# Kernel optimization log

Hardware: AMD Instinct MI355X
Metric: run time of the kernel (lower is better)

Reference implementation:

```python
import jax, jax.numpy as jnp
import numpy as np

B = 2048; E = 6; H = 4; D = 128; DH = D // H
LTXT = 24; CS = 20; JD = 7; SD = 16; LD = 32; K = 2
NLB = 4; NLD = 3; VOCAB = 512; DFF = 4 * D


def _ln(x, s, b, eps=1e-5):
    m = x.mean(-1, keepdims=True)
    v = ((x - m) ** 2).mean(-1, keepdims=True)
    return (x - m) * jax.lax.rsqrt(v + eps) * s + b


def _mha(xq, xkv, Wqkv, bqkv, Wo, bo, key_pad=None):
    # torch nn.MultiheadAttention, batch_first, eval (no dropout)
    Wq, Wk, Wv = jnp.split(Wqkv, 3, axis=-1)
    bq, bk, bv = jnp.split(bqkv, 3)
    Bc, Lq, _ = xq.shape
    Lk = xkv.shape[1]
    q = (xq @ Wq + bq).reshape(Bc, Lq, H, DH)
    k = (xkv @ Wk + bk).reshape(Bc, Lk, H, DH)
    v = (xkv @ Wv + bv).reshape(Bc, Lk, H, DH)
    s = jnp.einsum('bqhd,bkhd->bhqk', q, k) * (1.0 / DH ** 0.5)
    if key_pad is not None:
        s = jnp.where(key_pad[:, None, None, :], -1e9, s)
    a = jax.nn.softmax(s, axis=-1)
    o = jnp.einsum('bhqk,bkhd->bqhd', a, v).reshape(Bc, Lq, D)
    return o @ Wo + bo


def _sinusoidal_pe(L, d):
    pos = jnp.arange(L, dtype=jnp.float32)[:, None]
    div = jnp.exp(jnp.arange(0, d, 2, dtype=jnp.float32) * (-np.log(10000.0) / d))
    pe = jnp.zeros((L, d), jnp.float32)
    pe = pe.at[:, 0::2].set(jnp.sin(pos * div))
    return pe.at[:, 1::2].set(jnp.cos(pos * div))


def _forward(ids, state, tok_emb, pos_emb, bert_Wqkv, bert_bqkv, bert_Wo, bert_bo, bert_W1, bert_b1, bert_W2, bert_b2, bert_ln_s, bert_ln_b, bert_lnf_s, bert_lnf_b, se_W1, se_b1, se_W2, se_b2, se_ln_s, se_ln_b, r_W1, r_b1, r_W2, r_b2, r_ln_s, r_ln_b, gate_W, gate_b, exp_sp_W, exp_sp_b, exp_zp_W, exp_zp_b, exp_attn_Wqkv, exp_attn_bqkv, exp_attn_Wo, exp_attn_bo, exp_ln_s, exp_ln_b, exp_ff_W1, exp_ff_b1, exp_ff_W2, exp_ff_b2, exp_head_W, exp_head_b):
    Bc = ids.shape[0]
    gelu = lambda t: jax.nn.gelu(t, approximate=False)
    # ---- MiniBERT (post-LN encoder) ----
    pad = ids == 0  # PAD token
    x = tok_emb[ids] + pos_emb[None]  # [B,24,128]
    for l in range(NLB):
        a = _mha(x, x, bert_Wqkv[l], bert_bqkv[l], bert_Wo[l], bert_bo[l], pad)
        x = _ln(x + a, bert_ln_s[l, 0], bert_ln_b[l, 0])
        h = gelu(x @ bert_W1[l] + bert_b1[l]) @ bert_W2[l] + bert_b2[l]
        x = _ln(x + h, bert_ln_s[l, 1], bert_ln_b[l, 1])
    intent = _ln(x, bert_lnf_s, bert_lnf_b)[:, 0]  # CLS embedding [B,128]
    # ---- StateEncoder (MLP + LN) ----
    semb = _ln(gelu(state @ se_W1 + se_b1) @ se_W2 + se_b2, se_ln_s, se_ln_b)
    # ---- FusionRouter: top-k gating ----
    fused = _ln(gelu(jnp.concatenate([intent, semb], -1) @ r_W1 + r_b1) @ r_W2 + r_b2, r_ln_s, r_ln_b)
    logits = fused @ gate_W + gate_b  # [B,6]
    all_probs = jax.nn.softmax(logits, axis=-1)
    tv, ti = jax.lax.top_k(logits, K)
    weights = jax.nn.softmax(tv, axis=-1)  # [B,2]
    # ---- ACTExperts, inference path (z = 0) ----
    qpe = _sinusoidal_pe(CS, D)
    z = jnp.zeros((Bc, LD), state.dtype)

    def one_expert(sp_W, sp_b, zp_W, zp_b, aW, ab, oW, ob, lns, lnb, fW1, fb1, fW2, fb2, hW, hb):
        mem = jnp.stack([state @ sp_W + sp_b, z @ zp_W + zp_b], axis=1)  # [B,2,128]
        xq = jnp.broadcast_to(qpe[None], (Bc, CS, D))
        for l in range(NLD):  # norm_first decoder layers, relu FFN
            xn = _ln(xq, lns[l, 0], lnb[l, 0])
            xq = xq + _mha(xn, xn, aW[l, 0], ab[l, 0], oW[l, 0], ob[l, 0])
            xn = _ln(xq, lns[l, 1], lnb[l, 1])
            xq = xq + _mha(xn, mem, aW[l, 1], ab[l, 1], oW[l, 1], ob[l, 1])
            xn = _ln(xq, lns[l, 2], lnb[l, 2])
            xq = xq + jax.nn.relu(xn @ fW1[l] + fb1[l]) @ fW2[l] + fb2[l]
        return xq @ hW + hb  # [B,20,7]

    outs = jax.vmap(one_expert)(exp_sp_W, exp_sp_b, exp_zp_W, exp_zp_b, exp_attn_Wqkv, exp_attn_bqkv, exp_attn_Wo, exp_attn_bo, exp_ln_s, exp_ln_b, exp_ff_W1, exp_ff_b1, exp_ff_W2, exp_ff_b2, exp_head_W, exp_head_b)  # [E,B,20,7]
    # scatter top-k weights to a dense [B,E] gate and combine expert outputs
    w_full = jnp.zeros((Bc, E), logits.dtype).at[jnp.arange(Bc)[:, None], ti].add(weights)
    return jnp.einsum('be,ebtj->btj', w_full, outs)


def setup_inputs() -> dict:
    key = jax.random.key(0)
    it = iter(jax.random.split(key, 64))
    w = lambda *shape: jax.random.normal(next(it), shape, jnp.float32) * 0.05
    inp = {}
    inp['ids'] = jax.random.randint(next(it), (B, LTXT), 0, VOCAB, dtype=jnp.int32)
    inp['state'] = jax.random.normal(next(it), (B, SD), jnp.float32)
    inp['tok_emb'] = w(VOCAB, D).at[0].set(0.0)  # padding_idx=0
    inp['pos_emb'] = w(LTXT, D)
    inp['bert_Wqkv'] = w(NLB, D, 3 * D); inp['bert_bqkv'] = jnp.zeros((NLB, 3 * D))
    inp['bert_Wo'] = w(NLB, D, D); inp['bert_bo'] = jnp.zeros((NLB, D))
    inp['bert_W1'] = w(NLB, D, DFF); inp['bert_b1'] = jnp.zeros((NLB, DFF))
    inp['bert_W2'] = w(NLB, DFF, D); inp['bert_b2'] = jnp.zeros((NLB, D))
    inp['bert_ln_s'] = jnp.ones((NLB, 2, D)); inp['bert_ln_b'] = jnp.zeros((NLB, 2, D))
    inp['bert_lnf_s'] = jnp.ones((D,)); inp['bert_lnf_b'] = jnp.zeros((D,))
    inp['se_W1'] = w(SD, D); inp['se_b1'] = jnp.zeros((D,))
    inp['se_W2'] = w(D, D); inp['se_b2'] = jnp.zeros((D,))
    inp['se_ln_s'] = jnp.ones((D,)); inp['se_ln_b'] = jnp.zeros((D,))
    inp['r_W1'] = w(2 * D, D); inp['r_b1'] = jnp.zeros((D,))
    inp['r_W2'] = w(D, D); inp['r_b2'] = jnp.zeros((D,))
    inp['r_ln_s'] = jnp.ones((D,)); inp['r_ln_b'] = jnp.zeros((D,))
    inp['gate_W'] = w(D, E) * 10.0  # non-degenerate routing (source inits zeros)
    inp['gate_b'] = jnp.zeros((E,))
    inp['exp_sp_W'] = w(E, SD, D); inp['exp_sp_b'] = jnp.zeros((E, D))
    inp['exp_zp_W'] = w(E, LD, D); inp['exp_zp_b'] = jnp.zeros((E, D))
    inp['exp_attn_Wqkv'] = w(E, NLD, 2, D, 3 * D); inp['exp_attn_bqkv'] = jnp.zeros((E, NLD, 2, 3 * D))
    inp['exp_attn_Wo'] = w(E, NLD, 2, D, D); inp['exp_attn_bo'] = jnp.zeros((E, NLD, 2, D))
    inp['exp_ln_s'] = jnp.ones((E, NLD, 3, D)); inp['exp_ln_b'] = jnp.zeros((E, NLD, 3, D))
    inp['exp_ff_W1'] = w(E, NLD, D, DFF); inp['exp_ff_b1'] = jnp.zeros((E, NLD, DFF))
    inp['exp_ff_W2'] = w(E, NLD, DFF, D); inp['exp_ff_b2'] = jnp.zeros((E, NLD, D))
    inp['exp_head_W'] = w(E, D, JD); inp['exp_head_b'] = jnp.zeros((E, JD))
    return inp


def reference(ids, state, tok_emb, pos_emb, bert_Wqkv, bert_bqkv, bert_Wo, bert_bo, bert_W1, bert_b1, bert_W2, bert_b2, bert_ln_s, bert_ln_b, bert_lnf_s, bert_lnf_b, se_W1, se_b1, se_W2, se_b2, se_ln_s, se_ln_b, r_W1, r_b1, r_W2, r_b2, r_ln_s, r_ln_b, gate_W, gate_b, exp_sp_W, exp_sp_b, exp_zp_W, exp_zp_b, exp_attn_Wqkv, exp_attn_bqkv, exp_attn_Wo, exp_attn_bo, exp_ln_s, exp_ln_b, exp_ff_W1, exp_ff_b1, exp_ff_W2, exp_ff_b2, exp_head_W, exp_head_b):
    return _forward(ids, state, tok_emb, pos_emb, bert_Wqkv, bert_bqkv, bert_Wo, bert_bo, bert_W1, bert_b1, bert_W2, bert_b2, bert_ln_s, bert_ln_b, bert_lnf_s, bert_lnf_b, se_W1, se_b1, se_W2, se_b2, se_ln_s, se_ln_b, r_W1, r_b1, r_W2, r_b2, r_ln_s, r_ln_b, gate_W, gate_b, exp_sp_W, exp_sp_b, exp_zp_W, exp_zp_b, exp_attn_Wqkv, exp_attn_bqkv, exp_attn_Wo, exp_attn_bo, exp_ln_s, exp_ln_b, exp_ff_W1, exp_ff_b1, exp_ff_W2, exp_ff_b2, exp_head_W, exp_head_b)
```

## Files before the change

kernel.cpp:

```cpp
#include <hip/hip_runtime.h>
#include <math.h>

#define DEVI __device__ __forceinline__

namespace {

constexpr int Bn   = 2048;
constexpr int En   = 6;
constexpr int Hn   = 4;
constexpr int Dn   = 128;
constexpr int DHn  = 32;
constexpr int LTn  = 24;
constexpr int CSn  = 20;
constexpr int JDn  = 7;
constexpr int SDn  = 16;
constexpr int NLBn = 4;
constexpr int NLDn = 3;
constexpr int DFFn = 512;
constexpr float INV_SQRT_DH = 0.17677669529663687f;

constexpr int PAIRS  = 4096;
constexpr int MPMAX  = PAIRS * 20 + En * 128;
constexpr int NBGMAX = PAIRS * 20 / 128 + En;
constexpr int GEXP_OFF = 64;
// ... 253 lines not shown
    for (int q = 0; q < 4; ++q) {
      s1[q] = v[0][q] + v[1][q];
      s2[q] = v[0][q] * v[0][q] + v[1][q] * v[1][q];
    }
#pragma unroll
    for (int o = 1; o < 16; o <<= 1)
#pragma unroll
      for (int q = 0; q < 4; ++q) { s1[q] += __shfl_xor(s1[q], o); s2[q] += __shfl_xor(s2[q], o); }
    if (r0 == 0)
#pragma unroll
      for (int q = 0; q < 4; ++q) { red[g * 4 + q][wv][0] = s1[q]; red[g * 4 + q][wv][1] = s2[q]; }
    __syncthreads();
#pragma unroll
    for (int q = 0; q < 4; ++q) {
      const int r = g * 4 + q;
      const float t1 = red[r][0][0] + red[r][1][0] + red[r][2][0] + red[r][3][0];
      const float t2 = red[r][0][1] + red[r][1][1] + red[r][2][1] + red[r][3][1];
      const float m  = t1 * (1.f / 128.f);
      const float rs = rsqrtf(t2 * (1.f / 128.f) - m * m + 1e-5f);
      const int row = mtg * 16 + r;
#pragma unroll
      for (int i = 0; i < 2; ++i) {
        const int col = (wv * 2 + i) * 16 + r0;
        const float o = (v[i][q] - m) * rs * gs[col] + gb[col];
        X[(size_t)row * 128 + col] = o;
        short hh, ll; split2(o, hh, ll);
        const size_t pk = apos(row, col, 4);
        OAh[pk] = hh; OAl[pk] = ll;
      }
    }
    __syncthreads();
  }
}

__global__ __launch_bounds__(256) void bw1_kernel(
    const short* __restrict__ Ah, const short* __restrict__ Al,
    const short* __restrict__ Bp, const float* __restrict__ bias,
    short* __restrict__ Hh, short* __restrict__ Hl)
{
  const int mt0 = (int)blockIdx.x * 4;
  const int nc  = (int)blockIdx.y;
  const int lane = (int)threadIdx.x & 63, wv = (int)threadIdx.x >> 6;
  const int r0 = lane & 15, g = lane >> 4;
  short8 bh[2][4], bl[2][4];
#pragma unroll
  for (int i = 0; i < 2; ++i)
#pragma unroll
    for (int kt = 0; kt < 4; ++kt) {
      const short* tb = Bp + (((size_t)(nc * 8 + wv * 2 + i) * 4 + kt) << 10);
      bh[i][kt] = *reinterpret_cast<const short8*>(tb + lane * 8);
      bl[i][kt] = *reinterpret_cast<const short8*>(tb + 512 + lane * 8);
    }
#pragma unroll 2
  for (int mt = 0; mt < 4; ++mt) {
    const int mtg = mt0 + mt;
    short8 ah[4], al[4];
#pragma unroll
    for (int kt = 0; kt < 4; ++kt) {
      ah[kt] = *reinterpret_cast<const short8*>(Ah + (((size_t)mtg * 4 + kt) * 64 + lane) * 8);
      al[kt] = *reinterpret_cast<const short8*>(Al + (((size_t)mtg * 4 + kt) * 64 + lane) * 8);
    }
#pragma unroll
    for (int i = 0; i < 2; ++i) {
      f32x4v c = {0.f, 0.f, 0.f, 0.f};
#pragma unroll
      for (int kt = 0; kt < 4; ++kt) {
        c = __builtin_amdgcn_mfma_f32_16x16x32_bf16(ah[kt], bh[i][kt], c, 0, 0, 0);
        c = __builtin_amdgcn_mfma_f32_16x16x32_bf16(al[kt], bh[i][kt], c, 0, 0, 0);
        c = __builtin_amdgcn_mfma_f32_16x16x32_bf16(ah[kt], bl[i][kt], c, 0, 0, 0);
      }
      const int col = nc * 128 + (wv * 2 + i) * 16 + r0;
      const float bb = bias[col];
#pragma unroll
      for (int q = 0; q < 4; ++q) {
        const int row = mtg * 16 + g * 4 + q;
        short hh, ll; split2(geluf(c[q] + bb), hh, ll);
        const size_t pk = apos(row, col, 16);
        Hh[pk] = hh; Hl[pk] = ll;
      }
    }
  }
}

__global__ __launch_bounds__(512) void bw2a_kernel(
    const short* __restrict__ Hh, const short* __restrict__ Hl,
    const short* __restrict__ Bp, const float* __restrict__ bias,
    float* __restrict__ X)
{
  const int mt0 = (int)blockIdx.x * 4;
  const int lane = (int)threadIdx.x & 63, wv = (int)threadIdx.x >> 6;
  const int r0 = lane & 15, g = lane >> 4;
  short8 bh[8], bl[8];
#pragma unroll
  for (int kk = 0; kk < 8; ++kk) {
    const short* tb = Bp + (((size_t)wv * 16 + kk) << 10);
    bh[kk] = *reinterpret_cast<const short8*>(tb + lane * 8);
    bl[kk] = *reinterpret_cast<const short8*>(tb + 512 + lane * 8);
  }
#pragma unroll 2
  for (int mt = 0; mt < 4; ++mt) {
    const int mtg = mt0 + mt;
    f32x4v c = {0.f, 0.f, 0.f, 0.f};
#pragma unroll
    for (int kk = 0; kk < 8; ++kk) {
      const short8 ah = *reinterpret_cast<const short8*>(Hh + (((size_t)mtg * 16 + kk) * 64 + lane) * 8);
      const short8 al = *reinterpret_cast<const short8*>(Hl + (((size_t)mtg * 16 + kk) * 64 + lane) * 8);
      c = __builtin_amdgcn_mfma_f32_16x16x32_bf16(ah, bh[kk], c, 0, 0, 0);
      c = __builtin_amdgcn_mfma_f32_16x16x32_bf16(al, bh[kk], c, 0, 0, 0);
      c = __builtin_amdgcn_mfma_f32_16x16x32_bf16(ah, bl[kk], c, 0, 0, 0);
    }
    const int col = wv * 16 + r0;
    const float bb = bias[col];
#pragma unroll
    for (int q = 0; q < 4; ++q)
      X[(size_t)(mtg * 16 + g * 4 + q) * 128 + col] += c[q] + bb;
  }
}

__global__ __launch_bounds__(512) void bw2b_kernel(
    const short* __restrict__ Hh, const short* __restrict__ Hl,
    const short* __restrict__ Bp, const float* __restrict__ gs,
    const float* __restrict__ gb, float* __restrict__ X,
    short* __restrict__ OAh, short* __restrict__ OAl)
{
  __shared__ float red[16][8][2];
  const int mt0 = (int)blockIdx.x * 4;
  const int lane = (int)threadIdx.x & 63, wv = (int)threadIdx.x >> 6;
  const int r0 = lane & 15, g = lane >> 4;
  short8 bh[8], bl[8];
#pragma unroll
  for (int kk = 0; kk < 8; ++kk) {
    const short* tb = Bp + (((size_t)wv * 16 + 8 + kk) << 10);
    bh[kk] = *reinterpret_cast<const short8*>(tb + lane * 8);
    bl[kk] = *reinterpret_cast<const short8*>(tb + 512 + lane * 8);
  }
  for (int mt = 0; mt < 4; ++mt) {
    const int mtg = mt0 + mt;
    f32x4v c = {0.f, 0.f, 0.f, 0.f};
#pragma unroll
    for (int kk = 0; kk < 8; ++kk) {
      const short8 ah = *reinterpret_cast<const short8*>(Hh + (((size_t)mtg * 16 + 8 + kk) * 64 + lane) * 8);
      const short8 al = *reinterpret_cast<const short8*>(Hl + (((size_t)mtg * 16 + 8 + kk) * 64 + lane) * 8);
      c = __builtin_amdgcn_mfma_f32_16x16x32_bf16(ah, bh[kk], c, 0, 0, 0);
      c = __builtin_amdgcn_mfma_f32_16x16x32_bf16(al, bh[kk], c, 0, 0, 0);
      c = __builtin_amdgcn_mfma_f32_16x16x32_bf16(ah, bl[kk], c, 0, 0, 0);
    }
    const int col = wv * 16 + r0;
    float v[4], s1[4], s2[4];
#pragma unroll
    for (int q = 0; q < 4; ++q) {
      const int row = mtg * 16 + g * 4 + q;
      v[q] = c[q] + X[(size_t)row * 128 + col];
      s1[q] = v[q]; s2[q] = v[q] * v[q];
    }
#pragma unroll
    for (int o = 1; o < 16; o <<= 1)
#pragma unroll
      for (int q = 0; q < 4; ++q) { s1[q] += __shfl_xor(s1[q], o); s2[q] += __shfl_xor(s2[q], o); }
    if (r0 == 0)
#pragma unroll
      for (int q = 0; q < 4; ++q) { red[g * 4 + q][wv][0] = s1[q]; red[g * 4 + q][wv][1] = s2[q]; }
    __syncthreads();
#pragma unroll
    for (int q = 0; q < 4; ++q) {
      const int r = g * 4 + q;
      float t1 = 0.f, t2 = 0.f;
#pragma unroll
      for (int w = 0; w < 8; ++w) { t1 += red[r][w][0]; t2 += red[r][w][1]; }
      const float m  = t1 * (1.f / 128.f);
      const float rs = rsqrtf(t2 * (1.f / 128.f) - m * m + 1e-5f);
      const int row = mtg * 16 + r;
      const float o = (v[q] - m) * rs * gs[col] + gb[col];
      X[(size_t)row * 128 + col] = o;
      short hh, ll; split2(o, hh, ll);
      const size_t pk = apos(row, col, 4);
      OAh[pk] = hh; OAl[pk] = ll;
    }
    __syncthreads();
  }
}

__global__ __launch_bounds__(256) void bintent_kernel(
    const float* __restrict__ X, const float* __restrict__ lnf_s,
    const float* __restrict__ lnf_b, float* __restrict__ intent)
{
  const int w = (int)threadIdx.x >> 6, lane = (int)threadIdx.x & 63;
  const int b = (int)blockIdx.x * 4 + w;
  const float* xr = X + (size_t)b * LTn * 128;
  const float a0 = xr[lane], a1 = xr[lane + 64];
  float s1 = a0 + a1, s2 = a0 * a0 + a1 * a1;
#pragma unroll
  for (int o = 32; o > 0; o >>= 1) { s1 += __shfl_xor(s1, o); s2 += __shfl_xor(s2, o); }
  const float m  = s1 * (1.f / 128.f);
  const float rs = rsqrtf(s2 * (1.f / 128.f) - m * m + 1e-5f);
  intent[b * 128 + lane]      = (a0 - m) * rs * lnf_s[lane]      + lnf_b[lane];
  intent[b * 128 + lane + 64] = (a1 - m) * rs * lnf_s[lane + 64] + lnf_b[lane + 64];
}

struct RouterP {
  const float* state; const float* intent;
  const float* se_W1; const float* se_b1; const float* se_W2; const float* se_b2;
  const float* se_ln_s; const float* se_ln_b;
  const float* r_W1; const float* r_b1; const float* r_W2; const float* r_b2;
  const float* r_ln_s; const float* r_ln_b;
  const float* gate_W; const float* gate_b;
  int* ridx; float* rwgt;
};

DEVI void ln128(float* x, const float* gs, const float* gb, float* red)
{
  const int c = (int)threadIdx.x;
  const float a = x[c];
  float s1 = a, s2 = a * a;
#pragma unroll
  for (int o = 32; o > 0; o >>= 1) { s1 += __shfl_xor(s1, o); s2 += __shfl_xor(s2, o); }
  const int wid = c >> 6;
  if ((c & 63) == 0) { red[wid * 2] = s1; red[wid * 2 + 1] = s2; }
  __syncthreads();
  s1 = red[0] + red[2]; s2 = red[1] + red[3];
  const float m  = s1 * (1.f / 128.f);
  const float rs = rsqrtf(s2 * (1.f / 128.f) - m * m + 1e-5f);
  __syncthreads();
  x[c] = (a - m) * rs * gs[c] + gb[c];
}

DEVI float dot128i(const float* __restrict__ h, const float* __restrict__ W,
                   const int c, const int wstr)
{
  float a0 = 0.f, a1 = 0.f, a2 = 0.f, a3 = 0.f;
#pragma unroll 8
  for (int k = 0; k < 128; k += 4) {
    a0 = fmaf(h[k + 0], W[(k + 0) * wstr + c], a0);
    a1 = fmaf(h[k + 1], W[(k + 1) * wstr + c], a1);
    a2 = fmaf(h[k + 2], W[(k + 2) * wstr + c], a2);
    a3 = fmaf(h[k + 3], W[(k + 3) * wstr + c], a3);
// ... 151 lines not shown
__global__ __launch_bounds__(256) void compose_kernel(
    const float* __restrict__ sp_W, const float* __restrict__ sp_b,
    const float* __restrict__ zp_b, const float* __restrict__ aW,
    const float* __restrict__ ab,
    float* __restrict__ C, float* __restrict__ k0c, float* __restrict__ k1c)
{
  const int li = (int)blockIdx.x;
  const int ex = li / NLDn;
  const int c2 = (int)threadIdx.x;
  const float* W   = aW + (size_t)(li * 2 + 1) * Dn * 384 + Dn;
  const float* bb  = ab + (size_t)(li * 2 + 1) * 384 + Dn;
  const float* spw = sp_W + ex * SDn * Dn;
  const float* spb = sp_b + ex * Dn;
  const float* zpb = zp_b + ex * Dn;
  float acc[SDn];
#pragma unroll
  for (int k = 0; k < SDn; ++k) acc[k] = 0.f;
  float a0 = 0.f, a1 = 0.f;
  for (int d = 0; d < Dn; ++d) {
    const float w = W[(size_t)d * 384 + c2];
#pragma unroll
    for (int k = 0; k < SDn; ++k) acc[k] = fmaf(spw[k * Dn + d], w, acc[k]);
    a0 = fmaf(spb[d], w, a0);
    a1 = fmaf(zpb[d], w, a1);
  }
#pragma unroll
  for (int k = 0; k < SDn; ++k) C[((size_t)li * SDn + k) * 256 + c2] = acc[k];
  k0c[li * 256 + c2] = bb[c2] + a0;
  k1c[li * 256 + c2] = bb[c2] + a1;
}

template<int NTW, int EPI, bool HASB>
__global__ __launch_bounds__(256) void gemm_k128(
    const short* __restrict__ A, const short* __restrict__ Bb, const int strideB,
    const float* __restrict__ biasb, const int strideBias, const int ntOff,
    short* __restrict__ OutBf, const int obstr, short* __restrict__ OutP,
    const float* __restrict__ lnsA, const float* __restrict__ lnbA, const int subOff,
    float* __restrict__ X, const int* __restrict__ sch)
{
  __shared__ float red[16][4][2];
  const int k = (int)blockIdx.x;
  if (k >= sch[0]) return;
  const int ex  = sch[GEXP_OFF + k];
  const int mt0 = sch[GMT_OFF + k];
  const short* Bp = Bb + (size_t)ex * strideB;
  const float* bias = biasb + (size_t)ex * strideBias;
  const float* gs = (EPI == 4) ? lnsA + ex * (NLDn * 3 * 128) + subOff : nullptr;
  const float* gb = (EPI == 4) ? lnbA + ex * (NLDn * 3 * 128) + subOff : nullptr;
  const int lane = (int)threadIdx.x & 63, wv = (int)threadIdx.x >> 6;
  const int r0 = lane & 15, g = lane >> 4;
  short8 bf[NTW][4];
#pragma unroll
  for (int i = 0; i < NTW; ++i)
#pragma unroll
    for (int kt = 0; kt < 4; ++kt)
      bf[i][kt] = *reinterpret_cast<const short8*>(
          Bp + (((size_t)(ntOff + wv * NTW + i) * 4 + kt) * 64 + lane) * 8);
  for (int mt = 0; mt < 8; ++mt) {
    short8 a[4];
#pragma unroll
    for (int kt = 0; kt < 4; ++kt)
      a[kt] = *reinterpret_cast<const short8*>(
          A + (((size_t)(mt0 + mt) * 4 + kt) * 64 + lane) * 8);
    float v[NTW][4];
#pragma unroll
    for (int i = 0; i < NTW; ++i) {
      f32x4v c = {0.f, 0.f, 0.f, 0.f};
#pragma unroll
      for (int kt = 0; kt < 4; ++kt)
        c = __builtin_amdgcn_mfma_f32_16x16x32_bf16(a[kt], bf[i][kt], c, 0, 0, 0);
      const int colL = (wv * NTW + i) * 16 + r0;
      const float bb = HASB ? bias[colL] : 0.f;
      const int rowB = (mt0 + mt) * 16 + g * 4;
#pragma unroll
      for (int q = 0; q < 4; ++q) {
        const int row = rowB + q;
        const float val = c[q] + bb;
        if (EPI == 0) {
          OutBf[(size_t)row * obstr + colL] = f2bf(val);
        } else if (EPI == 3) {
          const float rv = fmaxf(val, 0.f);
          const int j = colL >> 3, kt2 = j >> 2, g2 = j & 3;
          const int lp = g2 * 16 + (row & 15);
          OutP[(((size_t)(row >> 4) * 8 + kt2) * 64 + lp) * 8 + (colL & 7)] = f2bf(rv);
        } else {
          v[i][q] = val + X[(size_t)row * 128 + colL];
        }
      }
    }
    if (EPI == 4) {
      static_assert(EPI != 4 || NTW == 2, "fused LN requires NTW==2");
      float s1[4], s2[4];
#pragma unroll
      for (int q = 0; q < 4; ++q) {
        s1[q] = v[0][q] + v[1][q];
        s2[q] = v[0][q] * v[0][q] + v[1][q] * v[1][q];
      }
#pragma unroll
      for (int o = 1; o < 16; o <<= 1)
#pragma unroll
        for (int q = 0; q < 4; ++q) { s1[q] += __shfl_xor(s1[q], o); s2[q] += __shfl_xor(s2[q], o); }
      if (r0 == 0)
#pragma unroll
        for (int q = 0; q < 4; ++q) { red[g * 4 + q][wv][0] = s1[q]; red[g * 4 + q][wv][1] = s2[q]; }
      __syncthreads();
#pragma unroll
      for (int q = 0; q < 4; ++q) {
        const int r = g * 4 + q;
        const float t1 = red[r][0][0] + red[r][1][0] + red[r][2][0] + red[r][3][0];
        const float t2 = red[r][0][1] + red[r][1][1] + red[r][2][1] + red[r][3][1];
        const float m  = t1 * (1.f / 128.f);
        const float rs = rsqrtf(t2 * (1.f / 128.f) - m * m + 1e-5f);
        const int row = (mt0 + mt) * 16 + r;
#pragma unroll
        for (int i = 0; i < 2; ++i) {
          const int col = (wv * 2 + i) * 16 + r0;
          const float o = (v[i][q] - m) * rs * gs[col] + gb[col];
          X[(size_t)row * 128 + col] = v[i][q];
          OutP[apos(row, col, 4)] = f2bf(o);
        }
      }
      __syncthreads();
    }
  }
}

template<bool HASB, bool DOLN>
__global__ __launch_bounds__(256) void gemm_k256(
    const short* __restrict__ A, const short* __restrict__ Bb, const int strideB,
    const float* __restrict__ biasb, const int strideBias, const int ktOff,
    float* __restrict__ X, short* __restrict__ OutP,
    const float* __restrict__ lnsA, const float* __restrict__ lnbA, const int subOff,
    const int* __restrict__ sch)
{
  __shared__ float red[16][4][2];
  const int k = (int)blockIdx.x;
  if (k >= sch[0]) return;
  const int ex  = sch[GEXP_OFF + k];
  const int mt0 = sch[GMT_OFF + k];
  const short* Bp = Bb + (size_t)ex * strideB;
  const float* bias = biasb + (size_t)ex * strideBias;
  const float* gs = DOLN ? lnsA + ex * (NLDn * 3 * 128) + subOff : nullptr;
  const float* gb = DOLN ? lnbA + ex * (NLDn * 3 * 128) + subOff : nullptr;
  const int lane = (int)threadIdx.x & 63, wv = (int)threadIdx.x >> 6;
  const int r0 = lane & 15, g = lane >> 4;
  short8 bf[2][8];
#pragma unroll
  for (int i = 0; i < 2; ++i)
#pragma unroll
    for (int kk = 0; kk < 8; ++kk)
      bf[i][kk] = *reinterpret_cast<const short8*>(
          Bp + (((size_t)(wv * 2 + i) * 16 + ktOff + kk) * 64 + lane) * 8);
  for (int mt = 0; mt < 8; ++mt) {
    short8 a[8];
#pragma unroll
    for (int kk = 0; kk < 8; ++kk)
      a[kk] = *reinterpret_cast<const short8*>(
          A + (((size_t)(mt0 + mt) * 8 + kk) * 64 + lane) * 8);
    float v[2][4];
#pragma unroll
    for (int i = 0; i < 2; ++i) {
      f32x4v c = {0.f, 0.f, 0.f, 0.f};
#pragma unroll
      for (int kk = 0; kk < 8; ++kk)
        c = __builtin_amdgcn_mfma_f32_16x16x32_bf16(a[kk], bf[i][kk], c, 0, 0, 0);
      const int colL = (wv * 2 + i) * 16 + r0;
      const float bb = HASB ? bias[colL] : 0.f;
      const int rowB = (mt0 + mt) * 16 + g * 4;
#pragma unroll
      for (int q = 0; q < 4; ++q) {
        const int row = rowB + q;
        if (DOLN) v[i][q] = c[q] + bb + X[(size_t)row * 128 + colL];
        else      X[(size_t)row * 128 + colL] += c[q] + bb;
      }
    }
    if (DOLN) {
      float s1[4], s2[4];
#pragma unroll
      for (int q = 0; q < 4; ++q) {
        s1[q] = v[0][q] + v[1][q];
        s2[q] = v[0][q] * v[0][q] + v[1][q] * v[1][q];
      }
#pragma unroll
      for (int o = 1; o < 16; o <<= 1)
#pragma unroll
        for (int q = 0; q < 4; ++q) { s1[q] += __shfl_xor(s1[q], o); s2[q] += __shfl_xor(s2[q], o); }
      if (r0 == 0)
#pragma unroll
        for (int q = 0; q < 4; ++q) { red[g * 4 + q][wv][0] = s1[q]; red[g * 4 + q][wv][1] = s2[q]; }
      __syncthreads();
#pragma unroll
      for (int q = 0; q < 4; ++q) {
        const int r = g * 4 + q;
        const float t1 = red[r][0][0] + red[r][1][0] + red[r][2][0] + red[r][3][0];
        const float t2 = red[r][0][1] + red[r][1][1] + red[r][2][1] + red[r][3][1];
        const float m  = t1 * (1.f / 128.f);
        const float rs = rsqrtf(t2 * (1.f / 128.f) - m * m + 1e-5f);
        const int row = (mt0 + mt) * 16 + r;
#pragma unroll
        for (int i = 0; i < 2; ++i) {
          const int col = (wv * 2 + i) * 16 + r0;
          const float o = (v[i][q] - m) * rs * gs[col] + gb[col];
          X[(size_t)row * 128 + col] = v[i][q];
          OutP[apos(row, col, 4)] = f2bf(o);
        }
      }
      __syncthreads();
    }
  }
}

__global__ __launch_bounds__(64) void sattn_kernel(
    const short* __restrict__ QKVb, const int* __restrict__ prow,
    short* __restrict__ ANP)
{
  __shared__ float qs[CSn * HSTR], ks[CSn * HSTR], vs[CSn * HSTR];
  __shared__ float att[CSn * CSn];
  const int i = (int)blockIdx.x, h = (int)blockIdx.y;
  const int tid = (int)threadIdx.x;
  const int row0 = prow[i];
  for (int u = tid; u < CSn * 12; u += 64) {
    const int il = u / 12, r = u % 12, which = r >> 2, d8 = r & 3;
    const short8 s = *reinterpret_cast<const short8*>(
        QKVb + (size_t)(row0 + il) * 384 + which * 128 + h * 32 + d8 * 8);
    float* dst = (which == 0 ? qs : which == 1 ? ks : vs) + il * HSTR + d8 * 8;
#pragma unroll
    for (int u8 = 0; u8 < 8; ++u8) dst[u8] = bf2f(s[u8]);
  }
  __syncthreads();
  for (int e = tid; e < CSn * CSn; e += 64) {
    const int ii = e / CSn, j = e % CSn;
    const float* qp = qs + ii * HSTR;
    const float* kp = ks + j * HSTR;
    float acc = 0.f;
#pragma unroll
    for (int d = 0; d < DHn; d += 4) {
      const float4 qa = *reinterpret_cast<const float4*>(qp + d);
      const float4 kb = *reinterpret_cast<const float4*>(kp + d);
      acc += qa.x * kb.x + qa.y * kb.y + qa.z * kb.z + qa.w * kb.w;
    }
    att[e] = acc * INV_SQRT_DH;
  }
  __syncthreads();
  if (tid < CSn) {
    float* row = att + tid * CSn;
    float m = row[0];
#pragma unroll 4
    for (int j = 1; j < CSn; ++j) m = fmaxf(m, row[j]);
    float s = 0.f;
#pragma unroll 4
    for (int j = 0; j < CSn; ++j) { const float ex = expf(row[j] - m); row[j] = ex; s += ex; }
    const float inv = 1.f / s;
#pragma unroll 4
    for (int j = 0; j < CSn; ++j) row[j] *= inv;
  }
  __syncthreads();
  for (int e = tid; e < CSn * 32; e += 64) {
    const int ii = e >> 5, c = e & 31;
    const float* arow = att + ii * CSn;
    float acc = 0.f;
#pragma unroll 4
    for (int j = 0; j < CSn; ++j) acc = fmaf(arow[j], vs[j * HSTR + c], acc);
    ANP[apos(row0 + ii, h * 32 + c, 4)] = f2bf(acc);
  }
}

__global__ __launch_bounds__(256) void cattn_kernel(
    const short* __restrict__ Qb, const float* __restrict__ state,
    const float* __restrict__ C, const float* __restrict__ k0c,
    const float* __restrict__ k1c, const int layer,
    const int* __restrict__ plist, const int* __restrict__ prow,
    const int* __restrict__ pexp, short* __restrict__ ANP)
{
  __shared__ float q[CSn * Dn];
  __shared__ float memkv[2 * 256];
  __shared__ float catt[2 * Hn * CSn];
  __shared__ float st[SDn];
  const int i = (int)blockIdx.x;
  const int ex = pexp[i];
  const int b = plist[i] >> 1;
  const int li = ex * NLDn + layer;
  const int row0 = prow[i];
  const int tid = (int)threadIdx.x;

  if (tid < SDn) st[tid] = state[b * SDn + tid];
  for (int e8 = tid; e8 < CSn * 16; e8 += 256) {
    const int il = e8 >> 4, c8 = e8 & 15;
    const short8 s = *reinterpret_cast<const short8*>(
        Qb + (size_t)(row0 + il) * 128 + c8 * 8);
    float* dst = q + il * Dn + c8 * 8;
// ... 112 lines not shown
  float* rwgt   = (float*)alloc(PAIRS * 4);
  short* pQ     = (short*)alloc((size_t)36 * 49152 * 2);
  short* pO     = (short*)alloc((size_t)36 * 16384 * 2);
  short* pF1    = (short*)alloc((size_t)18 * 65536 * 2);
  short* pF2    = (short*)alloc((size_t)18 * 65536 * 2);
  short* pbQ    = (short*)alloc((size_t)4 * 98304 * 2);
  short* pbO    = (short*)alloc((size_t)4 * 32768 * 2);
  short* pbW1   = (short*)alloc((size_t)4 * 131072 * 2);
  short* pbW2   = (short*)alloc((size_t)4 * 131072 * 2);
  int*   sch    = (int*)  alloc(2048 * 4);
  int*   plist  = (int*)  alloc(PAIRS * 4);
  int*   prow   = (int*)  alloc(PAIRS * 4);
  int*   pexp   = (int*)  alloc(PAIRS * 4);
  int*   ppos   = (int*)  alloc(PAIRS * 4);
  float* Cmat   = (float*)alloc((size_t)18 * SDn * 256 * 4);
  float* k0c    = (float*)alloc((size_t)18 * 256 * 4);
  float* k1c    = (float*)alloc((size_t)18 * 256 * 4);
  constexpr size_t ARENA_BYTES = 192806912;
  char* arena = alloc(ARENA_BYTES);
  if ((size_t)(cur - (char*)d_ws) > ws_size) return;

  float* Xb  = (float*)(arena);
  short* Ah  = (short*)(arena + 25165824);
  short* Al  = (short*)(arena + 37748736);
  float* SBb = (float*)(arena + 50331648);
  short* Hh  = (short*)(arena + 50331648);
  short* Hl  = (short*)(arena + 100663296);
  float* X2   = (float*)(arena);
  short* ANP  = (short*)(arena + 42336256);
  short* SBh  = (short*)(arena + 63504384);
  float* Rbuf = (float*)(arena + 190513152);

  qpe_kernel<<<dim3(10), dim3(256), 0, stream>>>(qpe);

  {
    const int tq = 36 * 6144;
    pack_kernel<<<dim3((tq + 255) / 256), dim3(256), 0, stream>>>(
        (const float*)d_in[34], pQ, 128, 384, tq);
    const int to = 36 * 2048;
    pack_kernel<<<dim3((to + 255) / 256), dim3(256), 0, stream>>>(
        (const float*)d_in[36], pO, 128, 128, to);
    const int t1c = 18 * 8192;
    pack_kernel<<<dim3((t1c + 255) / 256), dim3(256), 0, stream>>>(
        (const float*)d_in[40], pF1, 128, 512, t1c);
    const int t2c = 18 * 8192;
    pack_kernel<<<dim3((t2c + 255) / 256), dim3(256), 0, stream>>>(
        (const float*)d_in[42], pF2, 512, 128, t2c);
    const int bq = 4 * 6144;
    pack2_kernel<<<dim3((bq + 255) / 256), dim3(256), 0, stream>>>(
        (const float*)d_in[4], pbQ, 128, 384, bq);
    const int bo = 4 * 2048;
    pack2_kernel<<<dim3((bo + 255) / 256), dim3(256), 0, stream>>>(
        (const float*)d_in[6], pbO, 128, 128, bo);
    const int bw1 = 4 * 8192;
    pack2_kernel<<<dim3((bw1 + 255) / 256), dim3(256), 0, stream>>>(
        (const float*)d_in[8], pbW1, 128, 512, bw1);
    const int bw2 = 4 * 8192;
    pack2_kernel<<<dim3((bw2 + 255) / 256), dim3(256), 0, stream>>>(
        (const float*)d_in[10], pbW2, 512, 128, bw2);
    compose_kernel<<<dim3(En * NLDn), dim3(256), 0, stream>>>(
        (const float*)d_in[30], (const float*)d_in[31], (const float*)d_in[33],
        (const float*)d_in[34], (const float*)d_in[35], Cmat, k0c, k1c);
  }

  {
    const float* bq  = (const float*)d_in[5];
    const float* bo  = (const float*)d_in[7];
    const float* b1  = (const float*)d_in[9];
    const float* b2  = (const float*)d_in[11];
    const float* lns = (const float*)d_in[12];
    const float* lnb = (const float*)d_in[13];

    bembed_kernel<<<dim3(ROWSB / 16), dim3(256), 0, stream>>>(
        ids, tok_emb, pos_emb, Xb, Ah, Al);
    for (int l = 0; l < NLBn; ++l) {
      bqkv_kernel<<<dim3(ROWSB / 64, 3), dim3(256), 0, stream>>>(
          Ah, Al, pbQ + (size_t)l * 98304, bq + l * 384, SBb);
      battn_kernel<<<dim3(Bn, Hn), dim3(64), 0, stream>>>(SBb, ids, Ah, Al);
      bo_ln_kernel<<<dim3(ROWSB / 64), dim3(256), 0, stream>>>(
          Ah, Al, pbO + (size_t)l * 32768, bo + l * 128,
          lns + l * 256, lnb + l * 256, Xb, Ah, Al);
      bw1_kernel<<<dim3(ROWSB / 64, 4), dim3(256), 0, stream>>>(
          Ah, Al, pbW1 + (size_t)l * 131072, b1 + l * 512, Hh, Hl);
      bw2a_kernel<<<dim3(ROWSB / 64), dim3(512), 0, stream>>>(
          Hh, Hl, pbW2 + (size_t)l * 131072, b2 + l * 128, Xb);
      bw2b_kernel<<<dim3(ROWSB / 64), dim3(512), 0, stream>>>(
          Hh, Hl, pbW2 + (size_t)l * 131072,
          lns + l * 256 + 128, lnb + l * 256 + 128, Xb, Ah, Al);
    }
    bintent_kernel<<<dim3(Bn / 4), dim3(256), 0, stream>>>(
        Xb, (const float*)d_in[14], (const float*)d_in[15], intent);
  }

  {
    RouterP rp;
    rp.state = state; rp.intent = intent;
    rp.se_W1 = (const float*)d_in[16]; rp.se_b1 = (const float*)d_in[17];
    rp.se_W2 = (const float*)d_in[18]; rp.se_b2 = (const float*)d_in[19];
    rp.se_ln_s = (const float*)d_in[20]; rp.se_ln_b = (const float*)d_in[21];
    rp.r_W1 = (const float*)d_in[22]; rp.r_b1 = (const float*)d_in[23];
    rp.r_W2 = (const float*)d_in[24]; rp.r_b2 = (const float*)d_in[25];
    rp.r_ln_s = (const float*)d_in[26]; rp.r_ln_b = (const float*)d_in[27];
    rp.gate_W = (const float*)d_in[28]; rp.gate_b = (const float*)d_in[29];
    rp.ridx = ridx; rp.rwgt = rwgt;
    router_kernel<<<dim3(Bn), dim3(128), 0, stream>>>(rp);
  }

  const float* ab   = (const float*)d_in[35];
  const float* abo  = (const float*)d_in[37];
  const float* lnsA = (const float*)d_in[38];
  const float* lnbA = (const float*)d_in[39];
  const float* fb1A = (const float*)d_in[41];
  const float* fb2A = (const float*)d_in[43];
  const float* hW   = (const float*)d_in[44];
  const float* hB   = (const float*)d_in[45];

  {
    sched_kernel<<<dim3(1), dim3(256), 0, stream>>>(ridx, sch, plist, prow, pexp, ppos);
    xinit_kernel<<<dim3(MPMAX * 32 / 256), dim3(256), 0, stream>>>(qpe, sch, X2);
    ln_pack_kernel<<<dim3(MPMAX / 16), dim3(256), 0, stream>>>(
        X2, ANP, lnsA, lnbA, 0, sch);
    short* HP = SBh;
    for (int l = 0; l < NLDn; ++l) {
      gemm_k128<6, 0, true><<<dim3(NBGMAX), dim3(256), 0, stream>>>(
          ANP, pQ + (l * 2 + 0) * 49152, 294912,
          ab + (l * 2 + 0) * 384, 2304, 0,
          SBh, 384, nullptr, nullptr, nullptr, 0, nullptr, sch);
      sattn_kernel<<<dim3(PAIRS, Hn), dim3(64), 0, stream>>>(SBh, prow, ANP);
      gemm_k128<2, 4, true><<<dim3(NBGMAX), dim3(256), 0, stream>>>(
          ANP, pO + (l * 2 + 0) * 16384, 98304,
          abo + (l * 2 + 0) * 128, 768, 0,
          nullptr, 0, ANP, lnsA, lnbA, (l * 3 + 1) * 128, X2, sch);
      gemm_k128<2, 0, true><<<dim3(NBGMAX), dim3(256), 0, stream>>>(
          ANP, pQ + (l * 2 + 1) * 49152, 294912,
          ab + (l * 2 + 1) * 384, 2304, 0,
          SBh, 128, nullptr, nullptr, nullptr, 0, nullptr, sch);
      cattn_kernel<<<dim3(PAIRS), dim3(256), 0, stream>>>(
          SBh, state, Cmat, k0c, k1c, l, plist, prow, pexp, ANP);
      gemm_k128<2, 4, true><<<dim3(NBGMAX), dim3(256), 0, stream>>>(
          ANP, pO + (l * 2 + 1) * 16384, 98304,
          abo + (l * 2 + 1) * 128, 768, 0,
          nullptr, 0, ANP, lnsA, lnbA, (l * 3 + 2) * 128, X2, sch);
      gemm_k128<4, 3, true><<<dim3(NBGMAX), dim3(256), 0, stream>>>(
          ANP, pF1 + l * 65536, 196608,
          fb1A + l * 512 + 0 * 256, 1536, 0,
          nullptr, 0, HP, nullptr, nullptr, 0, nullptr, sch);
      gemm_k256<true, false><<<dim3(NBGMAX), dim3(256), 0, stream>>>(
          HP, pF2 + l * 65536, 196608, fb2A + l * 128, 384, 0,
          X2, nullptr, nullptr, nullptr, 0, sch);
      gemm_k128<4, 3, true><<<dim3(NBGMAX), dim3(256), 0, stream>>>(
          ANP, pF1 + l * 65536, 196608,
          fb1A + l * 512 + 1 * 256, 1536, 16,
          nullptr, 0, HP, nullptr, nullptr, 0, nullptr, sch);
      if (l < NLDn - 1) {
        gemm_k256<false, true><<<dim3(NBGMAX), dim3(256), 0, stream>>>(
            HP, pF2 + l * 65536, 196608, fb2A + l * 128, 384, 8,
            X2, ANP, lnsA, lnbA, ((l + 1) * 3 + 0) * 128, sch);
      } else {
        gemm_k256<false, false><<<dim3(NBGMAX), dim3(256), 0, stream>>>(
            HP, pF2 + l * 65536, 196608, fb2A + l * 128, 384, 8,
            X2, nullptr, nullptr, nullptr, 0, sch);
      }
    }
    head_kernel<<<dim3(PAIRS), dim3(256), 0, stream>>>(
        X2, plist, prow, pexp, rwgt, hW, hB, Rbuf);
    combine_kernel<<<dim3((Bn * 140 + 255) / 256), dim3(256), 0, stream>>>(
        Rbuf, ppos, (float*)d_out);
  }
}
```

Baseline: 1.714 ms.

## Fuse split-K FFN second GEMM halves into single kernels for BERT and experts

The BERT FFN down-projection was split into two kernels over K halves (one accumulating into X, one adding and applying LayerNorm); they are merged into one kernel that loops over both K halves while holding accumulators for four M tiles in registers. The expert FFN path gets the same treatment: the two K=256 GEMM launches become one K=512 kernel, and the first up-projection GEMM now writes into a wider 16-tile H buffer via an ntOff offset. This removes a launch and a full read-modify-write of X per layer, at the cost of more live accumulator registers and a reordered launch sequence.

Measured after the change: 1.688 ms. No clear change (-1.5%).

```diff
diff --git a/kernel.cpp b/kernel.cpp
--- a/kernel.cpp
+++ b/kernel.cpp
@@ -359,75 +359,52 @@
   }
 }
 
-__global__ __launch_bounds__(512) void bw2a_kernel(
+__global__ __launch_bounds__(512) void bw2_kernel(
     const short* __restrict__ Hh, const short* __restrict__ Hl,
     const short* __restrict__ Bp, const float* __restrict__ bias,
-    float* __restrict__ X)
-{
-  const int mt0 = (int)blockIdx.x * 4;
-  const int lane = (int)threadIdx.x & 63, wv = (int)threadIdx.x >> 6;
-  const int r0 = lane & 15, g = lane >> 4;
-  short8 bh[8], bl[8];
-#pragma unroll
-  for (int kk = 0; kk < 8; ++kk) {
-    const short* tb = Bp + (((size_t)wv * 16 + kk) << 10);
-    bh[kk] = *reinterpret_cast<const short8*>(tb + lane * 8);
-    bl[kk] = *reinterpret_cast<const short8*>(tb + 512 + lane * 8);
-  }
-#pragma unroll 2
-  for (int mt = 0; mt < 4; ++mt) {
-    const int mtg = mt0 + mt;
-    f32x4v c = {0.f, 0.f, 0.f, 0.f};
-#pragma unroll
-    for (int kk = 0; kk < 8; ++kk) {
-      const short8 ah = *reinterpret_cast<const short8*>(Hh + (((size_t)mtg * 16 + kk) * 64 + lane) * 8);
-      const short8 al = *reinterpret_cast<const short8*>(Hl + (((size_t)mtg * 16 + kk) * 64 + lane) * 8);
-      c = __builtin_amdgcn_mfma_f32_16x16x32_bf16(ah, bh[kk], c, 0, 0, 0);
-      c = __builtin_amdgcn_mfma_f32_16x16x32_bf16(al, bh[kk], c, 0, 0, 0);
-      c = __builtin_amdgcn_mfma_f32_16x16x32_bf16(ah, bl[kk], c, 0, 0, 0);
-    }
-    const int col = wv * 16 + r0;
-    const float bb = bias[col];
-#pragma unroll
-    for (int q = 0; q < 4; ++q)
-      X[(size_t)(mtg * 16 + g * 4 + q) * 128 + col] += c[q] + bb;
-  }
-}
-
-__global__ __launch_bounds__(512) void bw2b_kernel(
-    const short* __restrict__ Hh, const short* __restrict__ Hl,
-    const short* __restrict__ Bp, const float* __restrict__ gs,
-    const float* __restrict__ gb, float* __restrict__ X,
-    short* __restrict__ OAh, short* __restrict__ OAl)
+    const float* __restrict__ gs, const float* __restrict__ gb,
+    float* __restrict__ X, short* __restrict__ OAh, short* __restrict__ OAl)
 {
   __shared__ float red[16][8][2];
   const int mt0 = (int)blockIdx.x * 4;
   const int lane = (int)threadIdx.x & 63, wv = (int)threadIdx.x >> 6;
   const int r0 = lane & 15, g = lane >> 4;
-  short8 bh[8], bl[8];
-#pragma unroll
-  for (int kk = 0; kk < 8; ++kk) {
-    const short* tb = Bp + (((size_t)wv * 16 + 8 + kk) << 10);
-    bh[kk] = *reinterpret_cast<const short8*>(tb + lane * 8);
-    bl[kk] = *reinterpret_cast<const short8*>(tb + 512 + lane * 8);
-  }
+  f32x4v c[4];
+#pragma unroll
+  for (int mt = 0; mt < 4; ++mt) c[mt] = (f32x4v){0.f, 0.f, 0.f, 0.f};
+#pragma unroll
+  for (int half = 0; half < 2; ++half) {
+    short8 bh[8], bl[8];
+#pragma unroll
+    for (int kk = 0; kk < 8; ++kk) {
+      const short* tb = Bp + (((size_t)(wv * 16 + half * 8 + kk)) << 10);
+      bh[kk] = *reinterpret_cast<const short8*>(tb + lane * 8);
+      bl[kk] = *reinterpret_cast<const short8*>(tb + 512 + lane * 8);
+    }
+#pragma unroll
+    for (int mt = 0; mt < 4; ++mt) {
+      const int mtg = mt0 + mt;
+#pragma unroll
+      for (int kk = 0; kk < 8; ++kk) {
+        const short8 ah = *reinterpret_cast<const short8*>(
+            Hh + (((size_t)mtg * 16 + half * 8 + kk) * 64 + lane) * 8);
+        const short8 al = *reinterpret_cast<const short8*>(
+            Hl + (((size_t)mtg * 16 + half * 8 + kk) * 64 + lane) * 8);
+        c[mt] = __builtin_amdgcn_mfma_f32_16x16x32_bf16(ah, bh[kk], c[mt], 0, 0, 0);
+        c[mt] = __builtin_amdgcn_mfma_f32_16x16x32_bf16(al, bh[kk], c[mt], 0, 0, 0);
+        c[mt] = __builtin_amdgcn_mfma_f32_16x16x32_bf16(ah, bl[kk], c[mt], 0, 0, 0);
+      }
+    }
+  }
+  const int col = wv * 16 + r0;
+  const float bb = bias[col];
   for (int mt = 0; mt < 4; ++mt) {
     const int mtg = mt0 + mt;
-    f32x4v c = {0.f, 0.f, 0.f, 0.f};
-#pragma unroll
-    for (int kk = 0; kk < 8; ++kk) {
-      const short8 ah = *reinterpret_cast<const short8*>(Hh + (((size_t)mtg * 16 + 8 + kk) * 64 + lane) * 8);
-      const short8 al = *reinterpret_cast<const short8*>(Hl + (((size_t)mtg * 16 + 8 + kk) * 64 + lane) * 8);
-      c = __builtin_amdgcn_mfma_f32_16x16x32_bf16(ah, bh[kk], c, 0, 0, 0);
-      c = __builtin_amdgcn_mfma_f32_16x16x32_bf16(al, bh[kk], c, 0, 0, 0);
-      c = __builtin_amdgcn_mfma_f32_16x16x32_bf16(ah, bl[kk], c, 0, 0, 0);
-    }
-    const int col = wv * 16 + r0;
     float v[4], s1[4], s2[4];
 #pragma unroll
     for (int q = 0; q < 4; ++q) {
       const int row = mtg * 16 + g * 4 + q;
-      v[q] = c[q] + X[(size_t)row * 128 + col];
+      v[q] = c[mt][q] + bb + X[(size_t)row * 128 + col];
       s1[q] = v[q]; s2[q] = v[q] * v[q];
     }
 #pragma unroll
@@ -745,14 +722,14 @@
           const float rv = fmaxf(val, 0.f);
           const int j = colL >> 3, kt2 = j >> 2, g2 = j & 3;
           const int lp = g2 * 16 + (row & 15);
-          OutP[(((size_t)(row >> 4) * 8 + kt2) * 64 + lp) * 8 + (colL & 7)] = f2bf(rv);
+          OutP[(((size_t)(row >> 4) * 16 + (ntOff >> 1) + kt2) * 64 + lp) * 8 + (colL & 7)]
+              = f2bf(rv);
         } else {
           v[i][q] = val + X[(size_t)row * 128 + colL];
         }
       }
     }
     if (EPI == 4) {
-      static_assert(EPI != 4 || NTW == 2, "fused LN requires NTW==2");
       float s1[4], s2[4];
 #pragma unroll
       for (int q = 0; q < 4; ++q) {
@@ -788,10 +765,10 @@
   }
 }
 
-template<bool HASB, bool DOLN>
-__global__ __launch_bounds__(256) void gemm_k256(
+template<bool DOLN>
+__global__ __launch_bounds__(256) void gemm_k256f(
     const short* __restrict__ A, const short* __restrict__ Bb, const int strideB,
-    const float* __restrict__ biasb, const int strideBias, const int ktOff,
+    const float* __restrict__ biasb, const int strideBias,
     float* __restrict__ X, short* __restrict__ OutP,
     const float* __restrict__ lnsA, const float* __restrict__ lnbA, const int subOff,
     const int* __restrict__ sch)
@@ -807,68 +784,94 @@
   const float* gb = DOLN ? lnbA + ex * (NLDn * 3 * 128) + subOff : nullptr;
   const int lane = (int)threadIdx.x & 63, wv = (int)threadIdx.x >> 6;
   const int r0 = lane & 15, g = lane >> 4;
-  short8 bf[2][8];
-#pragma unroll
-  for (int i = 0; i < 2; ++i)
-#pragma unroll
-    for (int kk = 0; kk < 8; ++kk)
-      bf[i][kk] = *reinterpret_cast<const short8*>(
-          Bp + (((size_t)(wv * 2 + i) * 16 + ktOff + kk) * 64 + lane) * 8);
-  for (int mt = 0; mt < 8; ++mt) {
-    short8 a[8];
-#pragma unroll
-    for (int kk = 0; kk < 8; ++kk)
-      a[kk] = *reinterpret_cast<const short8*>(
-          A + (((size_t)(mt0 + mt) * 8 + kk) * 64 + lane) * 8);
-    float v[2][4];
-#pragma unroll
-    for (int i = 0; i < 2; ++i) {
-      f32x4v c = {0.f, 0.f, 0.f, 0.f};
-#pragma unroll
-      for (int kk = 0; kk < 8; ++kk)
-        c = __builtin_amdgcn_mfma_f32_16x16x32_bf16(a[kk], bf[i][kk], c, 0, 0, 0);
-      const int colL = (wv * 2 + i) * 16 + r0;
-      const float bb = HASB ? bias[colL] : 0.f;
-      const int rowB = (mt0 + mt) * 16 + g * 4;
-#pragma unroll
-      for (int q = 0; q < 4; ++q) {
-        const int row = rowB + q;
-        if (DOLN) v[i][q] = c[q] + bb + X[(size_t)row * 128 + colL];
-        else      X[(size_t)row * 128 + colL] += c[q] + bb;
-      }
-    }
-    if (DOLN) {
-      float s1[4], s2[4];
-#pragma unroll
-      for (int q = 0; q < 4; ++q) {
-        s1[q] = v[0][q] + v[1][q];
-        s2[q] = v[0][q] * v[0][q] + v[1][q] * v[1][q];
-      }
-#pragma unroll
-      for (int o = 1; o < 16; o <<= 1)
-#pragma unroll
-        for (int q = 0; q < 4; ++q) { s1[q] += __shfl_xor(s1[q], o); s2[q] += __shfl_xor(s2[q], o); }
-      if (r0 == 0)
-#pragma unroll
-        for (int q = 0; q < 4; ++q) { red[g * 4 + q][wv][0] = s1[q]; red[g * 4 + q][wv][1] = s2[q]; }
-      __syncthreads();
-#pragma unroll
-      for (int q = 0; q < 4; ++q) {
-        const int r = g * 4 + q;
-        const float t1 = red[r][0][0] + red[r][1][0] + red[r][2][0] + red[r][3][0];
-        const float t2 = red[r][0][1] + red[r][1][1] + red[r][2][1] + red[r][3][1];
-        const float m  = t1 * (1.f / 128.f);
-        const float rs = rsqrtf(t2 * (1.f / 128.f) - m * m + 1e-5f);
-        const int row = (mt0 + mt) * 16 + r;
+#pragma unroll
+  for (int mc = 0; mc < 2; ++mc) {
+    f32x4v c[4][2];
+#pragma unroll
+    for (int mtl = 0; mtl < 4; ++mtl)
+#pragma unroll
+      for (int i = 0; i < 2; ++i) c[mtl][i] = (f32x4v){0.f, 0.f, 0.f, 0.f};
+#pragma unroll
+    for (int half = 0; half < 2; ++half) {
+      short8 bf[2][8];
+#pragma unroll
+      for (int i = 0; i < 2; ++i)
+#pragma unroll
+        for (int kk = 0; kk < 8; ++kk)
+          bf[i][kk] = *reinterpret_cast<const short8*>(
+              Bp + (((size_t)(wv * 2 + i) * 16 + half * 8 + kk) * 64 + lane) * 8);
+#pragma unroll
+      for (int mtl = 0; mtl < 4; ++mtl) {
+        const int mtg = mt0 + mc * 4 + mtl;
+        short8 a[8];
+#pragma unroll
+        for (int kk = 0; kk < 8; ++kk)
+          a[kk] = *reinterpret_cast<const short8*>(
+              A + (((size_t)mtg * 16 + half * 8 + kk) * 64 + lane) * 8);
+#pragma unroll
+        for (int i = 0; i < 2; ++i)
+#pragma unroll
+          for (int kk = 0; kk < 8; ++kk)
+            c[mtl][i] = __builtin_amdgcn_mfma_f32_16x16x32_bf16(a[kk], bf[i][kk], c[mtl][i], 0, 0, 0);
+      }
+    }
+#pragma unroll
+    for (int mtl = 0; mtl < 4; ++mtl) {
+      const int mtg = mt0 + mc * 4 + mtl;
+      float v[2][4];
+#pragma unroll
+      for (int i = 0; i < 2; ++i) {
+        const int colL = (wv * 2 + i) * 16 + r0;
+        const float bb = bias[colL];
+#pragma unroll
+        for (int q = 0; q < 4; ++q) {
+          const int row = mtg * 16 + g * 4 + q;
+          v[i][q] = c[mtl][i][q] + bb + X[(size_t)row * 128 + colL];
+        }
+      }
+      if (DOLN) {
+        float s1[4], s2[4];
+#pragma unroll
+        for (int q = 0; q < 4; ++q) {
+          s1[q] = v[0][q] + v[1][q];
+          s2[q] = v[0][q] * v[0][q] + v[1][q] * v[1][q];
+        }
+#pragma unroll
+        for (int o = 1; o < 16; o <<= 1)
+#pragma unroll
+          for (int q = 0; q < 4; ++q) { s1[q] += __shfl_xor(s1[q], o); s2[q] += __shfl_xor(s2[q], o); }
+        if (r0 == 0)
+#pragma unroll
+          for (int q = 0; q < 4; ++q) { red[g * 4 + q][wv][0] = s1[q]; red[g * 4 + q][wv][1] = s2[q]; }
+        __syncthreads();
+#pragma unroll
+        for (int q = 0; q < 4; ++q) {
+          const int r = g * 4 + q;
+          const float t1 = red[r][0][0] + red[r][1][0] + red[r][2][0] + red[r][3][0];
+          const float t2 = red[r][0][1] + red[r][1][1] + red[r][2][1] + red[r][3][1];
+          const float m  = t1 * (1.f / 128.f);
+          const float rs = rsqrtf(t2 * (1.f / 128.f) - m * m + 1e-5f);
+          const int row = mtg * 16 + r;
+#pragma unroll
+          for (int i = 0; i < 2; ++i) {
+            const int col = (wv * 2 + i) * 16 + r0;
+            const float o = (v[i][q] - m) * rs * gs[col] + gb[col];
+            X[(size_t)row * 128 + col] = v[i][q];
+            OutP[apos(row, col, 4)] = f2bf(o);
+          }
+        }
+        __syncthreads();
+      } else {
 #pragma unroll
         for (int i = 0; i < 2; ++i) {
-          const int col = (wv * 2 + i) * 16 + r0;
-          const float o = (v[i][q] - m) * rs * gs[col] + gb[col];
-          X[(size_t)row * 128 + col] = v[i][q];
-          OutP[apos(row, col, 4)] = f2bf(o);
+          const int colL = (wv * 2 + i) * 16 + r0;
+#pragma unroll
+          for (int q = 0; q < 4; ++q) {
+            const int row = mtg * 16 + g * 4 + q;
+            X[(size_t)row * 128 + colL] = v[i][q];
+          }
         }
       }
-      __syncthreads();
     }
   }
 }
@@ -1147,10 +1150,8 @@
           lns + l * 256, lnb + l * 256, Xb, Ah, Al);
       bw1_kernel<<<dim3(ROWSB / 64, 4), dim3(256), 0, stream>>>(
           Ah, Al, pbW1 + (size_t)l * 131072, b1 + l * 512, Hh, Hl);
-      bw2a_kernel<<<dim3(ROWSB / 64), dim3(512), 0, stream>>>(
-          Hh, Hl, pbW2 + (size_t)l * 131072, b2 + l * 128, Xb);
-      bw2b_kernel<<<dim3(ROWSB / 64), dim3(512), 0, stream>>>(
-          Hh, Hl, pbW2 + (size_t)l * 131072,
+      bw2_kernel<<<dim3(ROWSB / 64), dim3(512), 0, stream>>>(
+          Hh, Hl, pbW2 + (size_t)l * 131072, b2 + l * 128,
           lns + l * 256 + 128, lnb + l * 256 + 128, Xb, Ah, Al);
     }
     bintent_kernel<<<dim3(Bn / 4), dim3(256), 0, stream>>>(
@@ -1210,20 +1211,17 @@
           ANP, pF1 + l * 65536, 196608,
           fb1A + l * 512 + 0 * 256, 1536, 0,
           nullptr, 0, HP, nullptr, nullptr, 0, nullptr, sch);
-      gemm_k256<true, false><<<dim3(NBGMAX), dim3(256), 0, stream>>>(
-          HP, pF2 + l * 65536, 196608, fb2A + l * 128, 384, 0,
-          X2, nullptr, nullptr, nullptr, 0, sch);
       gemm_k128<4, 3, true><<<dim3(NBGMAX), dim3(256), 0, stream>>>(
           ANP, pF1 + l * 65536, 196608,
           fb1A + l * 512 + 1 * 256, 1536, 16,
           nullptr, 0, HP, nullptr, nullptr, 0, nullptr, sch);
       if (l < NLDn - 1) {
-        gemm_k256<false, true><<<dim3(NBGMAX), dim3(256), 0, stream>>>(
-            HP, pF2 + l * 65536, 196608, fb2A + l * 128, 384, 8,
+        gemm_k256f<true><<<dim3(NBGMAX), dim3(256), 0, stream>>>(
+            HP, pF2 + l * 65536, 196608, fb2A + l * 128, 384,
             X2, ANP, lnsA, lnbA, ((l + 1) * 3 + 0) * 128, sch);
       } else {
-        gemm_k256<false, false><<<dim3(NBGMAX), dim3(256), 0, stream>>>(
-            HP, pF2 + l * 65536, 196608, fb2A + l * 128, 384, 8,
+        gemm_k256f<false><<<dim3(NBGMAX), dim3(256), 0, stream>>>(
+            HP, pF2 + l * 65536, 196608, fb2A + l * 128, 384,
             X2, nullptr, nullptr, nullptr, 0, sch);
       }
     }
```
